# Kernel optimization log

Hardware: AMD Instinct MI355X
Metric: run time of the kernel (lower is better)

Reference implementation:

```python
import jax, jax.numpy as jnp
import numpy as np

N = 10000        # nodes
E = 320000       # edges (avg degree 32)
W = 256          # width (assert width >= 256)
H = 8            # num_head (RESCALE_EDGE assumed (1,1) -> nhead=8, dhead=32)
D = W // H       # per-head dim
BOND = 33        # EMBED_BOND[0]
BAG = 3          # indices per edge bag
EPS_GN = 1e-5


def setup_inputs() -> dict:
    key = jax.random.key(0)
    ks = jax.random.split(key, 12)
    x = jax.random.normal(ks[0], (N, W), dtype=jnp.float32)
    edge_idx = jax.random.randint(ks[1], (2, E), 0, N)
    edge_attr = jax.random.randint(ks[2], (E, BAG), 0, BOND)
    # node in-degree wrt scatter target edge_idx[1], clamped to >= 1
    deg = jax.ops.segment_sum(jnp.ones((E,), jnp.float32), edge_idx[1], num_segments=N)
    deg = jnp.maximum(deg, 1.0)
    s = 1.0 / np.sqrt(W)
    W_src = jax.random.normal(ks[3], (W, W), dtype=jnp.float32) * s
    W_tgt = jax.random.normal(ks[4], (W, W), dtype=jnp.float32) * s
    emb = jax.random.normal(ks[5], (BOND, W), dtype=jnp.float32) * 0.02
    emb = emb.at[0].set(0.0)  # padding_idx=0 row is zeros
    sd = 1.0 / np.sqrt(D)
    W_gate = jax.random.normal(ks[6], (H, D, D), dtype=jnp.float32) * sd  # grouped conv1d k=1
    W_val = jax.random.normal(ks[7], (H, D, D), dtype=jnp.float32) * sd
    W_post = jax.random.normal(ks[8], (W, W), dtype=jnp.float32) * s
    deg_param = jnp.zeros((W,), jnp.float32) - 0.01  # DegreeLayer degree_init
    return {"x": x, "deg": deg, "edge_idx": edge_idx, "edge_attr": edge_attr,
            "W_src": W_src, "W_tgt": W_tgt, "emb": emb,
            "W_gate": W_gate, "W_val": W_val, "W_post": W_post,
            "deg_param": deg_param}


def reference(x, deg, edge_idx, edge_attr, W_src, W_tgt, emb, W_gate, W_val, W_post, deg_param):
    # src/tgt 1x1 Conv1d == per-node linear, then edge gather
    xs = x @ W_src.T                      # [N, W]
    xt = x @ W_tgt.T                      # [N, W]
    xx = xs[edge_idx[0]] + xt[edge_idx[1]]  # [E, W]

    # EmbeddingBag(mode='mean', padding_idx=0): padded entries excluded
    mask = (edge_attr != 0).astype(xx.dtype)            # [E, BAG]
    bag = jnp.einsum('ebc,eb->ec', emb[edge_attr], mask)  # [E, W]
    cnt = jnp.maximum(mask.sum(-1, keepdims=True), 1.0)
    gate_bias = bag / cnt

    # GroupNorm(H, W, affine=False) over [E, W, 1]
    xg = xx.reshape(-1, H, D)
    mu = xg.mean(-1, keepdims=True)
    var = xg.var(-1, keepdims=True)
    xn = (xg - mu) / jnp.sqrt(var + EPS_GN)              # [E, H, D]

    # gated grouped 1x1 convs (dropout is identity at eval)
    gin = xn + gate_bias.reshape(-1, H, D)
    gate = jax.nn.relu(jnp.einsum('ehd,hfd->ehf', gin, W_gate))
    val = jnp.einsum('ehd,hfd->ehf', xn, W_val)
    act = (gate * val).reshape(-1, W)                    # [E, W]
    out_e = act @ W_post.T                               # [E, W]

    # scatter-sum to nodes, then degree rescale
    agg = jax.ops.segment_sum(out_e, edge_idx[1], num_segments=x.shape[0])
    return jnp.power(deg[:, None], deg_param) * agg      # [N, W]
```

## Files before the change

kernel.cpp:

```cpp
#include <hip/hip_runtime.h>

#define WID 256
#define EPS_GN 1e-5f

typedef __bf16 v8bf __attribute__((ext_vector_type(8)));
typedef __bf16 v2bf __attribute__((ext_vector_type(2)));
typedef float  v4f  __attribute__((ext_vector_type(4)));

__device__ inline unsigned short f2b(float f) {
    unsigned int u = __builtin_bit_cast(unsigned int, f);
    unsigned int r = (u + 0x7fffu + ((u >> 16) & 1u)) >> 16;
    return (unsigned short)r;
}
__device__ inline float lo16(unsigned int u) { return __builtin_bit_cast(float, u << 16); }
__device__ inline float hi16(unsigned int u) { return __builtin_bit_cast(float, u & 0xffff0000u); }

#if __has_builtin(__builtin_amdgcn_cvt_pk_bf16_f32)
__device__ inline unsigned int pkbf(float a, float b) {
    v2bf r = __builtin_amdgcn_cvt_pk_bf16_f32(a, b);
    return __builtin_bit_cast(unsigned int, r);
}
#else
__device__ inline unsigned int pkbf(float a, float b) {
    return (unsigned int)f2b(a) | ((unsigned int)f2b(b) << 16);
}
#endif

#if __has_builtin(__builtin_amdgcn_fdot2_f32_bf16)
__device__ inline float pairsum(unsigned int u, float s) {
    v2bf p = __builtin_bit_cast(v2bf, u);
    v2bf ones = __builtin_bit_cast(v2bf, 0x3f803f80u);
    return __builtin_amdgcn_fdot2_f32_bf16(p, ones, s, false);
}
#else
__device__ inline float pairsum(unsigned int u, float s) {
    return s + lo16(u) + hi16(u);
}
#endif

__global__ void cast_k(const float* __restrict__ Wsrc, const float* __restrict__ Wtgt,
                       const float* __restrict__ Wp, const float* __restrict__ Wg,
                       const float* __restrict__ Wv, const float* __restrict__ emb,
                       unsigned short* __restrict__ Wsb, unsigned short* __restrict__ Wtb,
                       unsigned short* __restrict__ Wpb, unsigned short* __restrict__ Wgb,
                       unsigned short* __restrict__ Wvb, unsigned short* __restrict__ embWgT,
                       int* __restrict__ cnt, int N, int BOND) {
    int i = blockIdx.x * 256 + threadIdx.x;
    int gsz = gridDim.x * 256;
    for (int j = i; j < N; j += gsz) cnt[j] = 0;
    for (int j = i; j < 65536; j += gsz) {
        Wsb[j] = f2b(Wsrc[j]); Wtb[j] = f2b(Wtgt[j]); Wpb[j] = f2b(Wp[j]);
    }
    for (int j = i; j < 8192; j += gsz) { Wgb[j] = f2b(Wg[j]); Wvb[j] = f2b(Wv[j]); }
    for (int j = i; j < 16384; j += gsz) {
        int jr = j >> 6, k = j & 63;
        float sacc = 0.f;
        if (k < BOND) {
            int h = jr >> 5, f = jr & 31;
            const float* er = emb + (size_t)k * WID + h * 32;
            const float* wr = Wg + h * 1024 + f * 32;
#pragma unroll
            for (int d = 0; d < 32; d++) sacc += er[d] * wr[d];
        }
        embWgT[jr * 64 + k] = f2b(sacc);
    }
}

__global__ __launch_bounds__(256, 2)
void prepproj_k(const float* __restrict__ x, const unsigned short* __restrict__ Wsb,
                const unsigned short* __restrict__ Wtb, const int* __restrict__ eidx,
                unsigned short* __restrict__ xsb, unsigned short* __restrict__ xtb,
                int* __restrict__ cnt, float* __restrict__ aggact,
                int N, int E, int PB, int AUX) {
    __shared__ unsigned short ab[32 * 264];
    int t = threadIdx.x, b = blockIdx.x;

    if (b >= PB) {
        int atid = (b - PB) * 256 + t, asz = AUX * 256;
        {
            float4* ap = (float4*)aggact;
            int n4 = (N * WID) >> 2;
            for (int i = atid; i < n4; i += asz) ap[i] = make_float4(0.f, 0.f, 0.f, 0.f);
        }
        for (int i = atid; i < E; i += asz) atomicAdd(&cnt[eidx[E + i]], 1);
        return;
    }

    int n0 = b * 32;
#pragma unroll
    for (int ch = 0; ch < 8; ch++) {
        int flat = ch * 1024 + t * 4;
        int row = flat >> 8, col = flat & 255;
        int n = n0 + row;
        float4 v = (n < N) ? *(const float4*)&x[(size_t)n * WID + col]
                           : make_float4(0.f, 0.f, 0.f, 0.f);
        *(uint2*)&ab[row * 264 + col] = make_uint2(pkbf(v.x, v.y), pkbf(v.z, v.w));
    }
    __syncthreads();
    int w = t >> 6, lane = t & 63, m = lane & 15, kg = lane >> 4;
#pragma unroll
    for (int pass = 0; pass < 2; pass++) {
        const unsigned short* Wb = pass ? Wtb : Wsb;
        unsigned short* outp = pass ? xtb : xsb;
        v4f acc[2][4];
#pragma unroll
        for (int mt = 0; mt < 2; mt++)
#pragma unroll
            for (int nt = 0; nt < 4; nt++) acc[mt][nt] = (v4f){0.f, 0.f, 0.f, 0.f};
#pragma unroll
        for (int kt = 0; kt < 8; kt++) {
            int k0 = kt * 32 + kg * 8;
            v8bf a0 = *(const v8bf*)&ab[m * 264 + k0];
            v8bf a1 = *(const v8bf*)&ab[(16 + m) * 264 + k0];
#pragma unroll
            for (int nt = 0; nt < 4; nt++) {
                int j = w * 64 + nt * 16 + m;
                v8bf bfr = *(const v8bf*)&Wb[j * 256 + k0];
                acc[0][nt] = __builtin_amdgcn_mfma_f32_16x16x32_bf16(a0, bfr, acc[0][nt], 0, 0, 0);
                acc[1][nt] = __builtin_amdgcn_mfma_f32_16x16x32_bf16(a1, bfr, acc[1][nt], 0, 0, 0);
            }
        }
#pragma unroll
        for (int mt = 0; mt < 2; mt++)
#pragma unroll
            for (int r = 0; r < 4; r++) {
                int n = n0 + mt * 16 + kg * 4 + r;
                if (n < N)
#pragma unroll
                    for (int nt = 0; nt < 4; nt++)
                        outp[(size_t)n * WID + w * 64 + nt * 16 + m] = f2b(acc[mt][nt][r]);
            }
    }
}

__global__ void scan_k(const int* __restrict__ cnt, int* __restrict__ cur, int N) {
    __shared__ int buf[10240];
    __shared__ int part[1024];
    int t = threadIdx.x;
    int C = (N + 1023) >> 10;
    int M = C << 10;
    for (int i = t; i < M; i += 1024) buf[i] = (i < N) ? cnt[i] : 0;
    __syncthreads();
    int base0 = t * C;
    int s = 0;
    for (int i = 0; i < C; i++) s += buf[base0 + i];
    part[t] = s;
    __syncthreads();
    for (int d = 1; d < 1024; d <<= 1) {
        int v = (t >= d) ? part[t - d] : 0;
        __syncthreads();
        part[t] += v;
        __syncthreads();
    }
    int base = (t == 0) ? 0 : part[t - 1];
    for (int i = 0; i < C; i++) {
        int idx = base0 + i;
        int v = buf[idx];
        buf[idx] = base;
        base += v;
    }
    __syncthreads();
    for (int i = t; i < N; i += 1024) cur[i] = buf[i];
}

__global__ void scat_k(const int* __restrict__ eidx, int* __restrict__ cur,
                       int* __restrict__ perm, int E) {
    int i = blockIdx.x * 256 + threadIdx.x;
    if (i < E) { int p = atomicAdd(&cur[eidx[E + i]], 1); perm[p] = i; }
}

__global__ __launch_bounds__(256, 7)
void edge_k(const unsigned short* __restrict__ xsb, const unsigned short* __restrict__ xtb,
            const int* __restrict__ eidx, const int* __restrict__ eattr,
            const int* __restrict__ perm, const unsigned short* __restrict__ Wgb,
            const unsigned short* __restrict__ Wvb, const unsigned short* __restrict__ embWgT,
            float* __restrict__ aggact, int E, int NT, int PER) {
    __shared__ unsigned short xxb[8704];
    __shared__ unsigned short Mld[32 * 72];
    __shared__ int src_s[32], tgt_s[32];
    __shared__ int segmask_s;

    int tile = (blockIdx.x & 7) * PER + (blockIdx.x >> 3);
    if (tile >= NT) return;
    int t = threadIdx.x;
    int e0 = tile * 32;
    int ne = min(32, E - e0);

    {
        int tgtv = -1;
        if (t < 32) {
            int p = (t < ne) ? perm[e0 + t] : -1;
            src_s[t] = (p >= 0) ? eidx[p] : 0;
            tgtv = (p >= 0) ? eidx[E + p] : -1;
            tgt_s[t] = (tgtv >= 0) ? tgtv : 0;
            int a0 = 0, a1 = 0, a2 = 0;
            if (p >= 0) {
                const int* ap = eattr + (size_t)p * 3;
                a0 = ap[0]; a1 = ap[1]; a2 = ap[2];
            }
            unsigned int* Mr = (unsigned int*)&Mld[t * 72];
#pragma unroll
            for (int q = 0; q < 32; q++) Mr[q] = 0;
            int c = (a0 != 0) + (a1 != 0) + (a2 != 0);
            float inv = (p >= 0 && c > 0) ? 1.f / (float)c : 0.f;
            float wa = inv * (float)(1 + (a1 == a0) + (a2 == a0));
            float wb = inv * (float)(1 + (a2 == a1));
            Mld[t * 72 + a0] = f2b(wa);
            if (a1 != a0) Mld[t * 72 + a1] = f2b(wb);
            if (a2 != a0 && a2 != a1) Mld[t * 72 + a2] = f2b(inv);
        }
        if (t < 64) {
            int nxt = __shfl_down(tgtv, 1);
            bool flag = (t < ne) && ((t == ne - 1) || (nxt != tgtv));
            unsigned long long bal = __ballot(flag);
            if (t == 0) segmask_s = (int)(unsigned int)bal;
        }
    }
    __syncthreads();

    {
        int e = t >> 3, c = t & 7;
        int sn = src_s[e], g = tgt_s[e];
        bool live = (e < ne);
        const uint4* ps = (const uint4*)(xsb + (size_t)sn * WID);
        const uint4* pt = (const uint4*)(xtb + (size_t)g * WID);
        uint4 us[4], ut[4];
#pragma unroll
        for (int i = 0; i < 4; i++) { us[i] = ps[c + 8 * i]; ut[i] = pt[c + 8 * i]; }
        float v[4][8], sum[4], sq[4];
#pragma unroll
        for (int i = 0; i < 4; i++) {
            const unsigned int* au = (const unsigned int*)&us[i];
            const unsigned int* bu = (const unsigned int*)&ut[i];
            sum[i] = 0.f; sq[i] = 0.f;
#pragma unroll
            for (int q = 0; q < 4; q++) {
                float x0 = lo16(au[q]) + lo16(bu[q]);
                float x1 = hi16(au[q]) + hi16(bu[q]);
                if (!live) { x0 = 0.f; x1 = 0.f; }
                v[i][2 * q] = x0; v[i][2 * q + 1] = x1;
                sum[i] += x0 + x1;
                sq[i] += x0 * x0 + x1 * x1;
            }
        }
#pragma unroll
        for (int mask = 1; mask <= 2; mask <<= 1)
#pragma unroll
            for (int i = 0; i < 4; i++) {
                sum[i] += __shfl_xor(sum[i], mask);
                sq[i]  += __shfl_xor(sq[i], mask);
            }
#pragma unroll
        for (int i = 0; i < 4; i++) {
            float mu = sum[i] * (1.f / 32.f);
            float var = sq[i] * (1.f / 32.f) - mu * mu;
            float rs = rsqrtf(var + EPS_GN);
            float nmr = -mu * rs;
            unsigned int pk[4];
#pragma unroll
            for (int q = 0; q < 4; q++)
                pk[q] = pkbf(fmaf(v[i][2 * q], rs, nmr), fmaf(v[i][2 * q + 1], rs, nmr));
            *(uint4*)&xxb[e * 264 + (c + 8 * i) * 8] = make_uint4(pk[0], pk[1], pk[2], pk[3]);
        }
    }
    __syncthreads();

    {
        int w = t >> 6, lane = t & 63, m = lane & 15, kg = lane >> 4;
        v8bf axn[2][2], aM[2][2];
#pragma unroll
        for (int mt = 0; mt < 2; mt++) {
            int row = mt * 16 + m;
            axn[0][mt] = *(const v8bf*)&xxb[row * 264 + (w * 2 + 0) * 32 + kg * 8];
            axn[1][mt] = *(const v8bf*)&xxb[row * 264 + (w * 2 + 1) * 32 + kg * 8];
            aM[mt][0] = *(const v8bf*)&Mld[row * 72 + kg * 8];
            aM[mt][1] = *(const v8bf*)&Mld[row * 72 + 32 + kg * 8];
        }
        __syncthreads();
        v4f z = {0.f, 0.f, 0.f, 0.f};
#pragma unroll
        for (int hh = 0; hh < 2; hh++) {
            int h = w * 2 + hh;
#pragma unroll
            for (int nt = 0; nt < 2; nt++) {
                int fj = nt * 16 + m;
                int j = h * 32 + fj;
                v8bf bWg = *(const v8bf*)&Wgb[h * 1024 + fj * 32 + kg * 8];
                v8bf bWv = *(const v8bf*)&Wvb[h * 1024 + fj * 32 + kg * 8];
                v8bf bE0 = *(const v8bf*)&embWgT[j * 64 + kg * 8];
                v8bf bE1 = *(const v8bf*)&embWgT[j * 64 + 32 + kg * 8];
#pragma unroll
                for (int mt = 0; mt < 2; mt++) {
                    v4f cgm = __builtin_amdgcn_mfma_f32_16x16x32_bf16(axn[hh][mt], bWg, z, 0, 0, 0);
                    cgm = __builtin_amdgcn_mfma_f32_16x16x32_bf16(aM[mt][0], bE0, cgm, 0, 0, 0);
                    cgm = __builtin_amdgcn_mfma_f32_16x16x32_bf16(aM[mt][1], bE1, cgm, 0, 0, 0);
                    v4f cv = __builtin_amdgcn_mfma_f32_16x16x32_bf16(axn[hh][mt], bWv, z, 0, 0, 0);
                    float a0 = fmaxf(cgm[0], 0.f) * cv[0];
                    float a1 = fmaxf(cgm[1], 0.f) * cv[1];
                    float a2 = fmaxf(cgm[2], 0.f) * cv[2];
                    float a3 = fmaxf(cgm[3], 0.f) * cv[3];
                    int e0i = mt * 16 + kg * 4;
                    *(unsigned int*)&xxb[j * 34 + e0i]     = pkbf(a0, a1);
                    *(unsigned int*)&xxb[j * 34 + e0i + 2] = pkbf(a2, a3);
                }
            }
        }
    }
    __syncthreads();

    {
        unsigned int mask = (unsigned int)__builtin_amdgcn_readfirstlane(segmask_s);
        float sum = 0.f;
#pragma unroll
        for (int i = 0; i < 16; i++) {
            unsigned int r = *(const unsigned int*)&xxb[t * 34 + 2 * i];
            if (!((mask >> (2 * i)) & 1)) {
                sum = pairsum(r, sum);
                if ((mask >> (2 * i + 1)) & 1) {
                    int tg = __builtin_amdgcn_readfirstlane(tgt_s[2 * i + 1]);
                    atomicAdd(&aggact[(size_t)tg * WID + t], sum);
                    sum = 0.f;
                }
            } else {
                sum += lo16(r);
                int tg = __builtin_amdgcn_readfirstlane(tgt_s[2 * i]);
                atomicAdd(&aggact[(size_t)tg * WID + t], sum);
                sum = hi16(r);
                if ((mask >> (2 * i + 1)) & 1) {
                    int tg2 = __builtin_amdgcn_readfirstlane(tgt_s[2 * i + 1]);
                    atomicAdd(&aggact[(size_t)tg2 * WID + t], sum);
                    sum = 0.f;
                }
            }
        }
    }
}

__global__ __launch_bounds__(256, 2)
void post_k(const float* __restrict__ aggact, const unsigned short* __restrict__ Wpb,
            const float* __restrict__ deg, const float* __restrict__ dp,
            float* __restrict__ out, int N) {
    __shared__ unsigned short ab[32 * 264];
    __shared__ float degl[32];
    int t = threadIdx.x;
    int n0 = blockIdx.x * 32;
#pragma unroll
    for (int ch = 0; ch < 8; ch++) {
        int flat = ch * 1024 + t * 4;
        int row = flat >> 8, col = flat & 255;
        int n = n0 + row;
        float4 v = (n < N) ? *(const float4*)&aggact[(size_t)n * WID + col]
                           : make_float4(0.f, 0.f, 0.f, 0.f);
        *(uint2*)&ab[row * 264 + col] = make_uint2(pkbf(v.x, v.y), pkbf(v.z, v.w));
    }
    if (t < 32) {
        int n = n0 + t;
        degl[t] = (n < N) ? log2f(deg[n]) : 0.f;
    }
    __syncthreads();
    int w = t >> 6, lane = t & 63, m = lane & 15, kg = lane >> 4;
    v4f acc[2][4];
#pragma unroll
    for (int mt = 0; mt < 2; mt++)
#pragma unroll
        for (int nt = 0; nt < 4; nt++) acc[mt][nt] = (v4f){0.f, 0.f, 0.f, 0.f};
#pragma unroll
    for (int kt = 0; kt < 8; kt++) {
        int k0 = kt * 32 + kg * 8;
        v8bf a0 = *(const v8bf*)&ab[m * 264 + k0];
        v8bf a1 = *(const v8bf*)&ab[(16 + m) * 264 + k0];
#pragma unroll
        for (int nt = 0; nt < 4; nt++) {
            int j = w * 64 + nt * 16 + m;
            v8bf b = *(const v8bf*)&Wpb[j * 256 + k0];
            acc[0][nt] = __builtin_amdgcn_mfma_f32_16x16x32_bf16(a0, b, acc[0][nt], 0, 0, 0);
            acc[1][nt] = __builtin_amdgcn_mfma_f32_16x16x32_bf16(a1, b, acc[1][nt], 0, 0, 0);
        }
    }
    float dpv[4];
#pragma unroll
    for (int nt = 0; nt < 4; nt++) dpv[nt] = dp[w * 64 + nt * 16 + m];
#pragma unroll
    for (int mt = 0; mt < 2; mt++)
#pragma unroll
        for (int r = 0; r < 4; r++) {
            int row = mt * 16 + kg * 4 + r;
            int n = n0 + row;
            if (n < N) {
                float ld = degl[row];
#pragma unroll
                for (int nt = 0; nt < 4; nt++)
                    out[(size_t)n * WID + w * 64 + nt * 16 + m] =
                        exp2f(dpv[nt] * ld) * acc[mt][nt][r];
            }
        }
}

extern "C" void kernel_launch(void* const* d_in, const int* in_sizes, int n_in,
                              void* d_out, int out_size, void* d_ws, size_t ws_size,
                              hipStream_t stream) {
    const float* x    = (const float*)d_in[0];
    const float* deg  = (const float*)d_in[1];
    const int*   eidx = (const int*)d_in[2];
    const int*   eatt = (const int*)d_in[3];
    const float* Wsrc = (const float*)d_in[4];
    const float* Wtgt = (const float*)d_in[5];
    const float* emb  = (const float*)d_in[6];
    const float* Wg   = (const float*)d_in[7];
    const float* Wv   = (const float*)d_in[8];
    const float* Wp   = (const float*)d_in[9];
    const float* dp   = (const float*)d_in[10];
    int N = in_sizes[0] / WID;
    int E = in_sizes[2] / 2;
    int BOND = in_sizes[6] / WID;

    float* ws     = (float*)d_ws;
    float* aggact = ws;
    int*   cnt    = (int*)(aggact + (size_t)N * WID);
    int*   cur    = cnt + N;
    int*   perm   = cur + N;
    unsigned short* xsb = (unsigned short*)(perm + E);
    unsigned short* xtb = xsb + (size_t)N * WID;
    unsigned short* Wsb = xtb + (size_t)N * WID;
    unsigned short* Wtb = Wsb + 65536;
    unsigned short* Wpb = Wtb + 65536;
    unsigned short* Wgb = Wpb + 65536;
    unsigned short* Wvb = Wgb + 8192;
    unsigned short* embWgT = Wvb + 8192;

    int PB = (N + 31) / 32;
    int AUX = 128;
    int NT = (E + 31) / 32;
    int PER = (NT + 7) / 8;

    cast_k<<<320, 256, 0, stream>>>(Wsrc, Wtgt, Wp, Wg, Wv, emb,
                                    Wsb, Wtb, Wpb, Wgb, Wvb, embWgT, cnt, N, BOND);
    prepproj_k<<<PB + AUX, 256, 0, stream>>>(x, Wsb, Wtb, eidx, xsb, xtb, cnt, aggact,
                                             N, E, PB, AUX);
    scan_k<<<1, 1024, 0, stream>>>(cnt, cur, N);
    scat_k<<<(E + 255) / 256, 256, 0, stream>>>(eidx, cur, perm, E);
    edge_k<<<PER * 8, 256, 0, stream>>>(xsb, xtb, eidx, eatt, perm, Wgb, Wvb, embWgT,
                                        aggact, E, NT, PER);
    post_k<<<(N + 31) / 32, 256, 0, stream>>>(aggact, Wpb, deg, dp, (float*)d_out, N);
}
```

Measured before the change: 231.4 us.

## Fuse scan into projection kernel and split projection and post GEMM across more blocks

Degree counting and aggregate zeroing move into the weight-cast kernel, with cnt cleared by a memset. The 1024-thread scan kernel is folded into the projection launch as an extra 256-thread block, which removes one launch. The src and tgt projections now run in separate blocks (twice the grid), and post_k splits its output columns across two blocks in y, giving more parallelism at the cost of reloading x and the aggregate tile twice. The scan now runs on 256 threads with a longer serial loop per thread, and it runs concurrently with the projection blocks.

```diff
diff --git a/kernel.cpp b/kernel.cpp
--- a/kernel.cpp
+++ b/kernel.cpp
@@ -41,13 +41,14 @@
 __global__ void cast_k(const float* __restrict__ Wsrc, const float* __restrict__ Wtgt,
                        const float* __restrict__ Wp, const float* __restrict__ Wg,
                        const float* __restrict__ Wv, const float* __restrict__ emb,
+                       const int* __restrict__ eidx,
                        unsigned short* __restrict__ Wsb, unsigned short* __restrict__ Wtb,
                        unsigned short* __restrict__ Wpb, unsigned short* __restrict__ Wgb,
                        unsigned short* __restrict__ Wvb, unsigned short* __restrict__ embWgT,
-                       int* __restrict__ cnt, int N, int BOND) {
+                       int* __restrict__ cnt, float* __restrict__ aggact,
+                       int N, int E, int BOND) {
     int i = blockIdx.x * 256 + threadIdx.x;
     int gsz = gridDim.x * 256;
-    for (int j = i; j < N; j += gsz) cnt[j] = 0;
     for (int j = i; j < 65536; j += gsz) {
         Wsb[j] = f2b(Wsrc[j]); Wtb[j] = f2b(Wtgt[j]); Wpb[j] = f2b(Wp[j]);
     }
@@ -64,29 +65,54 @@
         }
         embWgT[jr * 64 + k] = f2b(sacc);
     }
+    {
+        float4* ap = (float4*)aggact;
+        int n4 = (N * WID) >> 2;
+        for (int j = i; j < n4; j += gsz) ap[j] = make_float4(0.f, 0.f, 0.f, 0.f);
+    }
+    for (int j = i; j < E; j += gsz) atomicAdd(&cnt[eidx[E + j]], 1);
 }
 
 __global__ __launch_bounds__(256, 2)
-void prepproj_k(const float* __restrict__ x, const unsigned short* __restrict__ Wsb,
-                const unsigned short* __restrict__ Wtb, const int* __restrict__ eidx,
-                unsigned short* __restrict__ xsb, unsigned short* __restrict__ xtb,
-                int* __restrict__ cnt, float* __restrict__ aggact,
-                int N, int E, int PB, int AUX) {
-    __shared__ unsigned short ab[32 * 264];
+void projscan_k(const float* __restrict__ x, const unsigned short* __restrict__ Wsb,
+                const unsigned short* __restrict__ Wtb, const int* __restrict__ cnt,
+                int* __restrict__ cur, unsigned short* __restrict__ xsb,
+                unsigned short* __restrict__ xtb, int N, int PB) {
+    __shared__ int sbuf[10496];
     int t = threadIdx.x, b = blockIdx.x;
 
-    if (b >= PB) {
-        int atid = (b - PB) * 256 + t, asz = AUX * 256;
-        {
-            float4* ap = (float4*)aggact;
-            int n4 = (N * WID) >> 2;
-            for (int i = atid; i < n4; i += asz) ap[i] = make_float4(0.f, 0.f, 0.f, 0.f);
-        }
-        for (int i = atid; i < E; i += asz) atomicAdd(&cnt[eidx[E + i]], 1);
+    if (b == 2 * PB) {
+        int C = (N + 255) >> 8;
+        int M = C << 8;
+        for (int i = t; i < M; i += 256) sbuf[i] = (i < N) ? cnt[i] : 0;
+        __syncthreads();
+        int base0 = t * C;
+        int s = 0;
+        for (int i = 0; i < C; i++) s += sbuf[base0 + i];
+        int* part = sbuf + 10240;
+        part[t] = s;
+        __syncthreads();
+        for (int d = 1; d < 256; d <<= 1) {
+            int v = (t >= d) ? part[t - d] : 0;
+            __syncthreads();
+            part[t] += v;
+            __syncthreads();
+        }
+        int base = (t == 0) ? 0 : part[t - 1];
+        for (int i = 0; i < C; i++) {
+            int idx = base0 + i;
+            int v = sbuf[idx];
+            sbuf[idx] = base;
+            base += v;
+        }
+        __syncthreads();
+        for (int i = t; i < N; i += 256) cur[i] = sbuf[i];
         return;
     }
 
-    int n0 = b * 32;
+    int pass = (b >= PB);
+    int n0 = (b - pass * PB) * 32;
+    unsigned short* ab = (unsigned short*)sbuf;
 #pragma unroll
     for (int ch = 0; ch < 8; ch++) {
         int flat = ch * 1024 + t * 4;
@@ -98,69 +124,36 @@
     }
     __syncthreads();
     int w = t >> 6, lane = t & 63, m = lane & 15, kg = lane >> 4;
-#pragma unroll
-    for (int pass = 0; pass < 2; pass++) {
-        const unsigned short* Wb = pass ? Wtb : Wsb;
-        unsigned short* outp = pass ? xtb : xsb;
-        v4f acc[2][4];
-#pragma unroll
-        for (int mt = 0; mt < 2; mt++)
-#pragma unroll
-            for (int nt = 0; nt < 4; nt++) acc[mt][nt] = (v4f){0.f, 0.f, 0.f, 0.f};
-#pragma unroll
-        for (int kt = 0; kt < 8; kt++) {
-            int k0 = kt * 32 + kg * 8;
-            v8bf a0 = *(const v8bf*)&ab[m * 264 + k0];
-            v8bf a1 = *(const v8bf*)&ab[(16 + m) * 264 + k0];
-#pragma unroll
-            for (int nt = 0; nt < 4; nt++) {
-                int j = w * 64 + nt * 16 + m;
-                v8bf bfr = *(const v8bf*)&Wb[j * 256 + k0];
-                acc[0][nt] = __builtin_amdgcn_mfma_f32_16x16x32_bf16(a0, bfr, acc[0][nt], 0, 0, 0);
-                acc[1][nt] = __builtin_amdgcn_mfma_f32_16x16x32_bf16(a1, bfr, acc[1][nt], 0, 0, 0);
-            }
-        }
-#pragma unroll
-        for (int mt = 0; mt < 2; mt++)
-#pragma unroll
-            for (int r = 0; r < 4; r++) {
-                int n = n0 + mt * 16 + kg * 4 + r;
-                if (n < N)
-#pragma unroll
-                    for (int nt = 0; nt < 4; nt++)
-                        outp[(size_t)n * WID + w * 64 + nt * 16 + m] = f2b(acc[mt][nt][r]);
-            }
-    }
-}
-
-__global__ void scan_k(const int* __restrict__ cnt, int* __restrict__ cur, int N) {
-    __shared__ int buf[10240];
-    __shared__ int part[1024];
-    int t = threadIdx.x;
-    int C = (N + 1023) >> 10;
-    int M = C << 10;
-    for (int i = t; i < M; i += 1024) buf[i] = (i < N) ? cnt[i] : 0;
-    __syncthreads();
-    int base0 = t * C;
-    int s = 0;
-    for (int i = 0; i < C; i++) s += buf[base0 + i];
-    part[t] = s;
-    __syncthreads();
-    for (int d = 1; d < 1024; d <<= 1) {
-        int v = (t >= d) ? part[t - d] : 0;
-        __syncthreads();
-        part[t] += v;
-        __syncthreads();
-    }
-    int base = (t == 0) ? 0 : part[t - 1];
-    for (int i = 0; i < C; i++) {
-        int idx = base0 + i;
-        int v = buf[idx];
-        buf[idx] = base;
-        base += v;
-    }
-    __syncthreads();
-    for (int i = t; i < N; i += 1024) cur[i] = buf[i];
+    const unsigned short* Wb = pass ? Wtb : Wsb;
+    unsigned short* outp = pass ? xtb : xsb;
+    v4f acc[2][4];
+#pragma unroll
+    for (int mt = 0; mt < 2; mt++)
+#pragma unroll
+        for (int nt = 0; nt < 4; nt++) acc[mt][nt] = (v4f){0.f, 0.f, 0.f, 0.f};
+#pragma unroll
+    for (int kt = 0; kt < 8; kt++) {
+        int k0 = kt * 32 + kg * 8;
+        v8bf a0 = *(const v8bf*)&ab[m * 264 + k0];
+        v8bf a1 = *(const v8bf*)&ab[(16 + m) * 264 + k0];
+#pragma unroll
+        for (int nt = 0; nt < 4; nt++) {
+            int j = w * 64 + nt * 16 + m;
+            v8bf bfr = *(const v8bf*)&Wb[j * 256 + k0];
+            acc[0][nt] = __builtin_amdgcn_mfma_f32_16x16x32_bf16(a0, bfr, acc[0][nt], 0, 0, 0);
+            acc[1][nt] = __builtin_amdgcn_mfma_f32_16x16x32_bf16(a1, bfr, acc[1][nt], 0, 0, 0);
+        }
+    }
+#pragma unroll
+    for (int mt = 0; mt < 2; mt++)
+#pragma unroll
+        for (int r = 0; r < 4; r++) {
+            int n = n0 + mt * 16 + kg * 4 + r;
+            if (n < N)
+#pragma unroll
+                for (int nt = 0; nt < 4; nt++)
+                    outp[(size_t)n * WID + w * 64 + nt * 16 + m] = f2b(acc[mt][nt][r]);
+        }
 }
 
 __global__ void scat_k(const int* __restrict__ eidx, int* __restrict__ cur,
@@ -344,6 +337,7 @@
     __shared__ float degl[32];
     int t = threadIdx.x;
     int n0 = blockIdx.x * 32;
+    int jbase = blockIdx.y * 128;
 #pragma unroll
     for (int ch = 0; ch < 8; ch++) {
         int flat = ch * 1024 + t * 4;
@@ -359,27 +353,27 @@
     }
     __syncthreads();
     int w = t >> 6, lane = t & 63, m = lane & 15, kg = lane >> 4;
-    v4f acc[2][4];
+    v4f acc[2][2];
 #pragma unroll
     for (int mt = 0; mt < 2; mt++)
 #pragma unroll
-        for (int nt = 0; nt < 4; nt++) acc[mt][nt] = (v4f){0.f, 0.f, 0.f, 0.f};
+        for (int nt = 0; nt < 2; nt++) acc[mt][nt] = (v4f){0.f, 0.f, 0.f, 0.f};
 #pragma unroll
     for (int kt = 0; kt < 8; kt++) {
         int k0 = kt * 32 + kg * 8;
         v8bf a0 = *(const v8bf*)&ab[m * 264 + k0];
         v8bf a1 = *(const v8bf*)&ab[(16 + m) * 264 + k0];
 #pragma unroll
-        for (int nt = 0; nt < 4; nt++) {
-            int j = w * 64 + nt * 16 + m;
+        for (int nt = 0; nt < 2; nt++) {
+            int j = jbase + w * 32 + nt * 16 + m;
             v8bf b = *(const v8bf*)&Wpb[j * 256 + k0];
             acc[0][nt] = __builtin_amdgcn_mfma_f32_16x16x32_bf16(a0, b, acc[0][nt], 0, 0, 0);
             acc[1][nt] = __builtin_amdgcn_mfma_f32_16x16x32_bf16(a1, b, acc[1][nt], 0, 0, 0);
         }
     }
-    float dpv[4];
-#pragma unroll
-    for (int nt = 0; nt < 4; nt++) dpv[nt] = dp[w * 64 + nt * 16 + m];
+    float dpv[2];
+#pragma unroll
+    for (int nt = 0; nt < 2; nt++) dpv[nt] = dp[jbase + w * 32 + nt * 16 + m];
 #pragma unroll
     for (int mt = 0; mt < 2; mt++)
 #pragma unroll
@@ -389,8 +383,8 @@
             if (n < N) {
                 float ld = degl[row];
 #pragma unroll
-                for (int nt = 0; nt < 4; nt++)
-                    out[(size_t)n * WID + w * 64 + nt * 16 + m] =
+                for (int nt = 0; nt < 2; nt++)
+                    out[(size_t)n * WID + jbase + w * 32 + nt * 16 + m] =
                         exp2f(dpv[nt] * ld) * acc[mt][nt][r];
             }
         }
@@ -429,17 +423,16 @@
     unsigned short* embWgT = Wvb + 8192;
 
     int PB = (N + 31) / 32;
-    int AUX = 128;
     int NT = (E + 31) / 32;
     int PER = (NT + 7) / 8;
 
-    cast_k<<<320, 256, 0, stream>>>(Wsrc, Wtgt, Wp, Wg, Wv, emb,
-                                    Wsb, Wtb, Wpb, Wgb, Wvb, embWgT, cnt, N, BOND);
-    prepproj_k<<<PB + AUX, 256, 0, stream>>>(x, Wsb, Wtb, eidx, xsb, xtb, cnt, aggact,
-                                             N, E, PB, AUX);
-    scan_k<<<1, 1024, 0, stream>>>(cnt, cur, N);
+    hipMemsetAsync(cnt, 0, (size_t)N * sizeof(int), stream);
+    cast_k<<<320, 256, 0, stream>>>(Wsrc, Wtgt, Wp, Wg, Wv, emb, eidx,
+                                    Wsb, Wtb, Wpb, Wgb, Wvb, embWgT, cnt, aggact,
+                                    N, E, BOND);
+    projscan_k<<<2 * PB + 1, 256, 0, stream>>>(x, Wsb, Wtb, cnt, cur, xsb, xtb, N, PB);
     scat_k<<<(E + 255) / 256, 256, 0, stream>>>(eidx, cur, perm, E);
     edge_k<<<PER * 8, 256, 0, stream>>>(xsb, xtb, eidx, eatt, perm, Wgb, Wvb, embWgT,
                                         aggact, E, NT, PER);
-    post_k<<<(N + 31) / 32, 256, 0, stream>>>(aggact, Wpb, deg, dp, (float*)d_out, N);
-}
+    post_k<<<dim3(PB, 2), 256, 0, stream>>>(aggact, Wpb, deg, dp, (float*)d_out, N);
+}
```

Result: slower. 237.6 us (+2.7%).

## Move degree count into cast kernel and fold scan into projection launch

Applied to the files above, without the earlier changes.

Target-degree counting moves from the auxiliary blocks of the projection kernel into the weight-cast kernel, and counters are zeroed with a memset. The separate single-block scan kernel is removed, and one extra block in the projection launch now computes the exclusive prefix sum. This drops one kernel launch and runs the scan alongside the projection GEMM. The scan block uses only 256 threads reading global counts with strided per-thread chunks, so it may be slow and could sit on the critical path.

```diff
diff --git a/kernel.cpp b/kernel.cpp
--- a/kernel.cpp
+++ b/kernel.cpp
@@ -41,13 +41,13 @@
 __global__ void cast_k(const float* __restrict__ Wsrc, const float* __restrict__ Wtgt,
                        const float* __restrict__ Wp, const float* __restrict__ Wg,
                        const float* __restrict__ Wv, const float* __restrict__ emb,
+                       const int* __restrict__ eidx,
                        unsigned short* __restrict__ Wsb, unsigned short* __restrict__ Wtb,
                        unsigned short* __restrict__ Wpb, unsigned short* __restrict__ Wgb,
                        unsigned short* __restrict__ Wvb, unsigned short* __restrict__ embWgT,
-                       int* __restrict__ cnt, int N, int BOND) {
+                       int* __restrict__ cnt, int E, int BOND) {
     int i = blockIdx.x * 256 + threadIdx.x;
     int gsz = gridDim.x * 256;
-    for (int j = i; j < N; j += gsz) cnt[j] = 0;
     for (int j = i; j < 65536; j += gsz) {
         Wsb[j] = f2b(Wsrc[j]); Wtb[j] = f2b(Wtgt[j]); Wpb[j] = f2b(Wp[j]);
     }
@@ -64,25 +64,43 @@
         }
         embWgT[jr * 64 + k] = f2b(sacc);
     }
+    for (int j = i; j < E; j += gsz) atomicAdd(&cnt[eidx[E + j]], 1);
 }
 
 __global__ __launch_bounds__(256, 2)
 void prepproj_k(const float* __restrict__ x, const unsigned short* __restrict__ Wsb,
-                const unsigned short* __restrict__ Wtb, const int* __restrict__ eidx,
-                unsigned short* __restrict__ xsb, unsigned short* __restrict__ xtb,
-                int* __restrict__ cnt, float* __restrict__ aggact,
-                int N, int E, int PB, int AUX) {
+                const unsigned short* __restrict__ Wtb, const int* __restrict__ cnt,
+                int* __restrict__ cur, unsigned short* __restrict__ xsb,
+                unsigned short* __restrict__ xtb, float* __restrict__ aggact,
+                int N, int PB, int AUX) {
     __shared__ unsigned short ab[32 * 264];
+    __shared__ int part[256];
     int t = threadIdx.x, b = blockIdx.x;
 
+    if (b == PB + AUX) {
+        int C = (N + 255) >> 8;
+        int s = 0;
+        for (int i = 0; i < C; i++) { int idx = t * C + i; if (idx < N) s += cnt[idx]; }
+        part[t] = s;
+        __syncthreads();
+        for (int d = 1; d < 256; d <<= 1) {
+            int v = (t >= d) ? part[t - d] : 0;
+            __syncthreads();
+            part[t] += v;
+            __syncthreads();
+        }
+        int base = (t == 0) ? 0 : part[t - 1];
+        for (int i = 0; i < C; i++) {
+            int idx = t * C + i;
+            if (idx < N) { cur[idx] = base; base += cnt[idx]; }
+        }
+        return;
+    }
     if (b >= PB) {
         int atid = (b - PB) * 256 + t, asz = AUX * 256;
-        {
-            float4* ap = (float4*)aggact;
-            int n4 = (N * WID) >> 2;
-            for (int i = atid; i < n4; i += asz) ap[i] = make_float4(0.f, 0.f, 0.f, 0.f);
-        }
-        for (int i = atid; i < E; i += asz) atomicAdd(&cnt[eidx[E + i]], 1);
+        float4* ap = (float4*)aggact;
+        int n4 = (N * WID) >> 2;
+        for (int i = atid; i < n4; i += asz) ap[i] = make_float4(0.f, 0.f, 0.f, 0.f);
         return;
     }
 
@@ -131,36 +149,6 @@
                         outp[(size_t)n * WID + w * 64 + nt * 16 + m] = f2b(acc[mt][nt][r]);
             }
     }
-}
-
-__global__ void scan_k(const int* __restrict__ cnt, int* __restrict__ cur, int N) {
-    __shared__ int buf[10240];
-    __shared__ int part[1024];
-    int t = threadIdx.x;
-    int C = (N + 1023) >> 10;
-    int M = C << 10;
-    for (int i = t; i < M; i += 1024) buf[i] = (i < N) ? cnt[i] : 0;
-    __syncthreads();
-    int base0 = t * C;
-    int s = 0;
-    for (int i = 0; i < C; i++) s += buf[base0 + i];
-    part[t] = s;
-    __syncthreads();
-    for (int d = 1; d < 1024; d <<= 1) {
-        int v = (t >= d) ? part[t - d] : 0;
-        __syncthreads();
-        part[t] += v;
-        __syncthreads();
-    }
-    int base = (t == 0) ? 0 : part[t - 1];
-    for (int i = 0; i < C; i++) {
-        int idx = base0 + i;
-        int v = buf[idx];
-        buf[idx] = base;
-        base += v;
-    }
-    __syncthreads();
-    for (int i = t; i < N; i += 1024) cur[i] = buf[i];
 }
 
 __global__ void scat_k(const int* __restrict__ eidx, int* __restrict__ cur,
@@ -433,13 +421,13 @@
     int NT = (E + 31) / 32;
     int PER = (NT + 7) / 8;
 
-    cast_k<<<320, 256, 0, stream>>>(Wsrc, Wtgt, Wp, Wg, Wv, emb,
-                                    Wsb, Wtb, Wpb, Wgb, Wvb, embWgT, cnt, N, BOND);
-    prepproj_k<<<PB + AUX, 256, 0, stream>>>(x, Wsb, Wtb, eidx, xsb, xtb, cnt, aggact,
-                                             N, E, PB, AUX);
-    scan_k<<<1, 1024, 0, stream>>>(cnt, cur, N);
+    hipMemsetAsync(cnt, 0, (size_t)N * sizeof(int), stream);
+    cast_k<<<320, 256, 0, stream>>>(Wsrc, Wtgt, Wp, Wg, Wv, emb, eidx,
+                                    Wsb, Wtb, Wpb, Wgb, Wvb, embWgT, cnt, E, BOND);
+    prepproj_k<<<PB + AUX + 1, 256, 0, stream>>>(x, Wsb, Wtb, cnt, cur, xsb, xtb, aggact,
+                                                 N, PB, AUX);
     scat_k<<<(E + 255) / 256, 256, 0, stream>>>(eidx, cur, perm, E);
     edge_k<<<PER * 8, 256, 0, stream>>>(xsb, xtb, eidx, eatt, perm, Wgb, Wvb, embWgT,
                                         aggact, E, NT, PER);
-    post_k<<<(N + 31) / 32, 256, 0, stream>>>(aggact, Wpb, deg, dp, (float*)d_out, N);
-}
+    post_k<<<PB, 256, 0, stream>>>(aggact, Wpb, deg, dp, (float*)d_out, N);
+}
```

Result: slower. 243.2 us (+5.1%).
